# Performance work log

Measured on AMD Instinct MI355X. Metric: run time of the kernel, lower is better.

## Reference

```python
import jax, jax.numpy as jnp
import numpy as np

N = 100000   # nodes
E = 600000   # edges
F_IN = 128
F_OUT = 128


def setup_inputs() -> dict:
    key = jax.random.key(0)
    k1, k2, k3, k4 = jax.random.split(key, 4)
    x = jax.random.normal(k1, (N, F_IN), dtype=jnp.float32)
    edge_index = jax.random.randint(k2, (2, E), 0, N, dtype=jnp.int32)
    edge_wt = jnp.ones((E,), dtype=jnp.float32)  # learnable param, init ones
    # GCNConv weight (glorot-ish scale) and bias
    weight = jax.random.normal(k3, (F_IN, F_OUT), dtype=jnp.float32) / np.sqrt(F_IN).astype(np.float32)
    bias = jnp.zeros((F_OUT,), dtype=jnp.float32)
    u = jax.random.normal(k4, (F_IN,), dtype=jnp.float32)  # spectral-norm power-iter buffer
    return {"x": x, "edge_index": edge_index, "edge_wt": edge_wt,
            "weight": weight, "bias": bias, "u": u}


def _l2norm(v):
    return v / (jnp.linalg.norm(v) + 1e-12)


def reference(x, edge_index, edge_wt, weight, bias, u):
    # --- spectral norm on GCNConv weight (one power iteration, torch semantics:
    # u, v are stop-gradiented buffers; sigma = u^T W v keeps grad wrt W) ---
    W_sg = jax.lax.stop_gradient(weight)
    v = _l2norm(W_sg.T @ jax.lax.stop_gradient(u))
    u1 = _l2norm(W_sg @ v)
    sigma = u1 @ (weight @ v)
    W_sn = weight / sigma

    # --- per-edge sigmoid-weighted GCNConv with self loops + symmetric norm ---
    w = jax.nn.sigmoid(edge_wt)                      # [E]
    row, col = edge_index[0], edge_index[1]
    loop = jnp.arange(N, dtype=edge_index.dtype)
    row_a = jnp.concatenate([row, loop])             # [E+N]
    col_a = jnp.concatenate([col, loop])
    w_a = jnp.concatenate([w, jnp.ones((N,), w.dtype)])  # self-loop weight 1

    deg = jax.ops.segment_sum(w_a, col_a, num_segments=N)   # [N]
    dinv = jnp.where(deg > 0, deg ** -0.5, 0.0)
    norm = dinv[row_a] * w_a * dinv[col_a]           # [E+N]

    xw = x @ W_sn                                    # [N, F_OUT]
    msgs = norm[:, None] * xw[row_a]                 # [E+N, F_OUT] gather
    out = jax.ops.segment_sum(msgs, col_a, num_segments=N) + bias  # scatter
    return out
```

## Files before the change

### kernel.cpp

```cpp
#include <hip/hip_runtime.h>
#include <math.h>

#define F 128

typedef __bf16 bf16_t;
typedef unsigned long long u64;
typedef __attribute__((ext_vector_type(8))) bf16_t bf16x8;
typedef __attribute__((ext_vector_type(4))) bf16_t bf16x4;
typedef __attribute__((ext_vector_type(4))) float floatx4;

#define DEG_SCALE 8388608.0f
#define DEG_INV   (1.0f / 8388608.0f)

__global__ __launch_bounds__(256) void init_spec_k(const float* __restrict__ W,
                                                   const float* __restrict__ u,
                                                   bf16_t* __restrict__ Wt,
                                                   u64* __restrict__ dc, int n) {
    if (blockIdx.x == 0) {
        __shared__ float sv[F];
        __shared__ float red[F];
        __shared__ float snorm;
        __shared__ float s_is;
        int t = threadIdx.x;
        float s = 0.f;
        if (t < F) {
            for (int i = 0; i < F; ++i) s += W[i * F + t] * u[i];
            red[t] = s * s;
        }
        __syncthreads();
        if (t == 0) {
            float a = 0.f;
            for (int i = 0; i < F; ++i) a += red[i];
            snorm = sqrtf(a);
        }
        __syncthreads();
        if (t < F) sv[t] = s / (snorm + 1e-12f);
        __syncthreads();
        float s2 = 0.f;
        if (t < F) {
            for (int j = 0; j < F; ++j) s2 += W[t * F + j] * sv[j];
            red[t] = s2 * s2;
        }
        __syncthreads();
        if (t == 0) {
            float a = 0.f;
            for (int i = 0; i < F; ++i) a += red[i];
            float nt = sqrtf(a);
            float sigma = a / (nt + 1e-12f);
            s_is = 1.0f / sigma;
        }
        __syncthreads();
        if (t < F) {
            float is = s_is;
            for (int nrow = 0; nrow < F; ++nrow)
                Wt[nrow * F + t] = (bf16_t)(W[t * F + nrow] * is);
        }
    } else {
        int i = (blockIdx.x - 1) * 256 + threadIdx.x;
        if (i < n) dc[i] = 0ULL;
    }
}

#define GBM 64
#define LDK 136
__global__ __launch_bounds__(256) void count_gemm_k(const int* __restrict__ col,
                                                    const float* __restrict__ wt,
                                                    u64* __restrict__ dc, int e_cnt,
                                                    const float* __restrict__ x,
                                                    const bf16_t* __restrict__ Wt,
                                                    bf16_t* __restrict__ xwh, int nrows,
                                                    int gGemm) {
    __shared__ bf16_t As[GBM * LDK];
    int b = blockIdx.x;
    if (b >= gGemm) {
        int e = (b - gGemm) * 256 + threadIdx.x;
        if (e < e_cnt) {
            int c = col[e];
            float w = 1.0f / (1.0f + expf(-wt[e]));
            u64 pkt = (1ULL << 32) | (u64)(unsigned)rintf(w * DEG_SCALE);
            atomicAdd(dc + c, pkt);
        }
        return;
    }
    int tid = threadIdx.x;
    int rowBase = b * GBM;

    for (int i = tid; i < GBM * 32; i += 256) {
        int r = i >> 5, c4 = (i & 31) * 4;
        float4 xv = make_float4(0.f, 0.f, 0.f, 0.f);
        if (rowBase + r < nrows) xv = *(const float4*)(x + (size_t)(rowBase + r) * F + c4);
        bf16x4 v;
        v.x = (bf16_t)xv.x; v.y = (bf16_t)xv.y; v.z = (bf16_t)xv.z; v.w = (bf16_t)xv.w;
        *(bf16x4*)(As + r * LDK + c4) = v;
    }
    __syncthreads();

    int wave = tid >> 6, lane = tid & 63;
    int l16 = lane & 15, q = lane >> 4;
    int mrow = wave * 16;

    floatx4 acc[8];
#pragma unroll
    for (int nt = 0; nt < 8; ++nt) acc[nt] = (floatx4){0.f, 0.f, 0.f, 0.f};

#pragma unroll
    for (int kt = 0; kt < 4; ++kt) {
        bf16x8 a = *(bf16x8*)(As + (mrow + l16) * LDK + kt * 32 + q * 8);
#pragma unroll
        for (int nt = 0; nt < 8; ++nt) {
            bf16x8 bb = *(const bf16x8*)(Wt + (size_t)(nt * 16 + l16) * F + kt * 32 + q * 8);
            acc[nt] = __builtin_amdgcn_mfma_f32_16x16x32_bf16(a, bb, acc[nt], 0, 0, 0);
        }
    }
    __syncthreads();

#pragma unroll
    for (int nt = 0; nt < 8; ++nt) {
#pragma unroll
        for (int r = 0; r < 4; ++r)
            As[(mrow + q * 4 + r) * LDK + nt * 16 + l16] = (bf16_t)acc[nt][r];
    }
    __syncthreads();

    for (int i = tid; i < GBM * 16; i += 256) {
        int r = i >> 4, c = (i & 15) * 8;
        if (rowBase + r < nrows)
            *(bf16x8*)(xwh + (size_t)(rowBase + r) * F + c) = *(bf16x8*)(As + r * LDK + c);
    }
}

#define STILE 1024
__global__ __launch_bounds__(256) void scan1_k(const u64* __restrict__ dc,
                                               int* __restrict__ bsum,
                                               float* __restrict__ dinv, int n) {
    __shared__ int red[256];
    int t = threadIdx.x;
    int base = blockIdx.x * STILE + t * 4;
    int s = 0;
    for (int i = 0; i < 4; ++i) {
        if (base + i < n) {
            u64 v = dc[base + i];
            s += (int)(v >> 32);
            float d = 1.0f + (float)(unsigned)(v & 0xFFFFFFFFULL) * DEG_INV;
            dinv[base + i] = 1.0f / sqrtf(d);
        }
    }
    red[t] = s;
    __syncthreads();
    for (int o = 128; o > 0; o >>= 1) { if (t < o) red[t] += red[t + o]; __syncthreads(); }
    if (t == 0) bsum[blockIdx.x] = red[0];
}

__global__ __launch_bounds__(256) void scan2_k(int* __restrict__ bsum, int g,
                                               int* __restrict__ offsets, int n) {
    int t = threadIdx.x;
    if (g <= 256) {
        __shared__ int s[256];
        int v = (t < g) ? bsum[t] : 0;
        s[t] = v;
        __syncthreads();
        for (int o = 1; o < 256; o <<= 1) {
            int val = s[t];
            int add = (t >= o) ? s[t - o] : 0;
            __syncthreads();
            s[t] = val + add;
            __syncthreads();
        }
        if (t < g) bsum[t] = s[t] - v;
        if (t == g - 1) offsets[n] = s[t];
    } else if (t == 0) {
        int acc = 0;
        for (int i = 0; i < g; ++i) { int v = bsum[i]; bsum[i] = acc; acc += v; }
        offsets[n] = acc;
    }
}

__global__ __launch_bounds__(256) void scan3_k(const u64* __restrict__ dc,
                                               const int* __restrict__ bsum,
                                               int* __restrict__ offsets,
                                               int* __restrict__ cursor, int n) {
    __shared__ int sc[256];
    int t = threadIdx.x;
    int base = blockIdx.x * STILE + t * 4;
    int v[4] = {0, 0, 0, 0};
    for (int i = 0; i < 4; ++i)
        if (base + i < n) v[i] = (int)(dc[base + i] >> 32);
    int ts = v[0] + v[1] + v[2] + v[3];
    sc[t] = ts;
    __syncthreads();
    for (int o = 1; o < 256; o <<= 1) {
        int val = sc[t];
        int add = (t >= o) ? sc[t - o] : 0;
        __syncthreads();
        sc[t] = val + add;
        __syncthreads();
    }
    int run = bsum[blockIdx.x] + sc[t] - ts;
    for (int i = 0; i < 4; ++i) {
        if (base + i < n) { offsets[base + i] = run; cursor[base + i] = run; }
        run += v[i];
    }
}

__global__ __launch_bounds__(256) void fill_k(const int* __restrict__ row,
                                              const int* __restrict__ col,
                                              const float* __restrict__ wt,
                                              const float* __restrict__ dinv,
                                              int* __restrict__ cursor,
                                              int2* __restrict__ edat, int e_cnt) {
    int e = blockIdx.x * 256 + threadIdx.x;
    if (e < e_cnt) {
        int r = row[e], c = col[e];
        float w = 1.0f / (1.0f + expf(-wt[e]));
        float nv = dinv[r] * w * dinv[c];
        int p = atomicAdd(cursor + c, 1);
        edat[p] = make_int2(r, __float_as_int(nv));
    }
}

template <int MODE>
__global__ __launch_bounds__(256) void gather_t(const int* __restrict__ offsets,
                                                const int2* __restrict__ edat,
                                                const float* __restrict__ dinv,
                                                const float* __restrict__ x,
                                                const bf16_t* __restrict__ xh,
                                                const float* __restrict__ bias,
                                                float* __restrict__ out, int n) {
    int node = blockIdx.x * 4 + (threadIdx.x >> 6);
    if (node >= n) return;
    int lane = threadIdx.x & 63;
    const float2* x2 = (const float2*)x;
    float dv = dinv[node];
    float2 acc;
    if (MODE) {
        unsigned vs = ((const unsigned*)(xh + (size_t)node * F))[lane];
        acc.x = dv * dv * __uint_as_float(vs << 16);
        acc.y = dv * dv * __uint_as_float(vs & 0xFFFF0000u);
    } else {
        float2 xv = x2[(size_t)node * 64 + lane];
        acc.x = dv * dv * xv.x;
        acc.y = dv * dv * xv.y;
    }
    int s = offsets[node], e = offsets[node + 1];
    for (int b = s; b < e; b += 64) {
        int cnt = min(64, e - b);
        int2 ed = make_int2(0, 0);
        if (lane < cnt) ed = edat[b + lane];
        int j = 0;
        for (; j + 4 <= cnt; j += 4) {
            int r0 = __shfl(ed.x, j + 0), r1 = __shfl(ed.x, j + 1);
            int r2 = __shfl(ed.x, j + 2), r3 = __shfl(ed.x, j + 3);
            float n0 = __int_as_float(__shfl(ed.y, j + 0));
            float n1 = __int_as_float(__shfl(ed.y, j + 1));
            float n2 = __int_as_float(__shfl(ed.y, j + 2));
            float n3 = __int_as_float(__shfl(ed.y, j + 3));
            if (MODE) {
                unsigned v0 = ((const unsigned*)(xh + (size_t)r0 * F))[lane];
                unsigned v1 = ((const unsigned*)(xh + (size_t)r1 * F))[lane];
                unsigned v2 = ((const unsigned*)(xh + (size_t)r2 * F))[lane];
                unsigned v3 = ((const unsigned*)(xh + (size_t)r3 * F))[lane];
                acc.x = fmaf(n0, __uint_as_float(v0 << 16), acc.x);
                acc.y = fmaf(n0, __uint_as_float(v0 & 0xFFFF0000u), acc.y);
                acc.x = fmaf(n1, __uint_as_float(v1 << 16), acc.x);
                acc.y = fmaf(n1, __uint_as_float(v1 & 0xFFFF0000u), acc.y);
                acc.x = fmaf(n2, __uint_as_float(v2 << 16), acc.x);
                acc.y = fmaf(n2, __uint_as_float(v2 & 0xFFFF0000u), acc.y);
                acc.x = fmaf(n3, __uint_as_float(v3 << 16), acc.x);
                acc.y = fmaf(n3, __uint_as_float(v3 & 0xFFFF0000u), acc.y);
            } else {
                float2 a0 = x2[(size_t)r0 * 64 + lane];
                float2 a1 = x2[(size_t)r1 * 64 + lane];
                float2 a2 = x2[(size_t)r2 * 64 + lane];
                float2 a3 = x2[(size_t)r3 * 64 + lane];
                acc.x = fmaf(n0, a0.x, acc.x); acc.y = fmaf(n0, a0.y, acc.y);
                acc.x = fmaf(n1, a1.x, acc.x); acc.y = fmaf(n1, a1.y, acc.y);
                acc.x = fmaf(n2, a2.x, acc.x); acc.y = fmaf(n2, a2.y, acc.y);
                acc.x = fmaf(n3, a3.x, acc.x); acc.y = fmaf(n3, a3.y, acc.y);
            }
        }
        for (; j < cnt; ++j) {
            int r = __shfl(ed.x, j);
            float nv = __int_as_float(__shfl(ed.y, j));
            if (MODE) {
                unsigned v = ((const unsigned*)(xh + (size_t)r * F))[lane];
                acc.x = fmaf(nv, __uint_as_float(v << 16), acc.x);
                acc.y = fmaf(nv, __uint_as_float(v & 0xFFFF0000u), acc.y);
            } else {
                float2 xr = x2[(size_t)r * 64 + lane];
                acc.x = fmaf(nv, xr.x, acc.x);
                acc.y = fmaf(nv, xr.y, acc.y);
            }
        }
    }
    if (MODE) {
        float2 bv = ((const float2*)bias)[lane];
        acc.x += bv.x;
        acc.y += bv.y;
    }
    ((float2*)out)[(size_t)node * 64 + lane] = acc;
}

__global__ __launch_bounds__(256) void gemm_mfma_k(float* __restrict__ io,
                                                   const bf16_t* __restrict__ Wt,
                                                   const float* __restrict__ bias,
                                                   int nrows) {
    __shared__ bf16_t As[GBM * LDK];
    int tid = threadIdx.x;
    int rowBase = blockIdx.x * GBM;

    for (int i = tid; i < GBM * 32; i += 256) {
        int r = i >> 5, c4 = (i & 31) * 4;
        float4 xv = make_float4(0.f, 0.f, 0.f, 0.f);
        if (rowBase + r < nrows) xv = *(const float4*)(io + (size_t)(rowBase + r) * F + c4);
        bf16x4 v;
        v.x = (bf16_t)xv.x; v.y = (bf16_t)xv.y; v.z = (bf16_t)xv.z; v.w = (bf16_t)xv.w;
        *(bf16x4*)(As + r * LDK + c4) = v;
    }
    __syncthreads();

    int wave = tid >> 6, lane = tid & 63;
    int l16 = lane & 15, q = lane >> 4;
    int mrow = wave * 16;

    floatx4 acc[8];
#pragma unroll
    for (int nt = 0; nt < 8; ++nt) acc[nt] = (floatx4){0.f, 0.f, 0.f, 0.f};

#pragma unroll
    for (int kt = 0; kt < 4; ++kt) {
        bf16x8 a = *(bf16x8*)(As + (mrow + l16) * LDK + kt * 32 + q * 8);
#pragma unroll
        for (int nt = 0; nt < 8; ++nt) {
            bf16x8 b = *(const bf16x8*)(Wt + (size_t)(nt * 16 + l16) * F + kt * 32 + q * 8);
            acc[nt] = __builtin_amdgcn_mfma_f32_16x16x32_bf16(a, b, acc[nt], 0, 0, 0);
        }
    }

#pragma unroll
    for (int nt = 0; nt < 8; ++nt) {
        int col = nt * 16 + l16;
        float bv = bias[col];
#pragma unroll
        for (int r = 0; r < 4; ++r) {
            int grow = rowBase + mrow + q * 4 + r;
            if (grow < nrows) io[(size_t)grow * F + col] = acc[nt][r] + bv;
        }
    }
}

extern "C" void kernel_launch(void* const* d_in, const int* in_sizes, int n_in,
                              void* d_out, int out_size, void* d_ws, size_t ws_size,
                              hipStream_t stream) {
    const float* x    = (const float*)d_in[0];
    const int*   ei   = (const int*)d_in[1];
    const float* ewt  = (const float*)d_in[2];
    const float* W    = (const float*)d_in[3];
    const float* bias = (const float*)d_in[4];
    const float* u    = (const float*)d_in[5];
    float* out = (float*)d_out;

    int n_nodes = in_sizes[0] / F;
    int e_cnt   = in_sizes[2];
    const int* row = ei;
    const int* col = ei + e_cnt;

    char* wsb = (char*)d_ws;
    float* dinv    = (float*)wsb;
    size_t off = ((size_t)n_nodes * 4 + 15) & ~(size_t)15;
    u64*   dc      = (u64*)(wsb + off);
    off += (size_t)n_nodes * 8;
    int*   offsets = (int*)(wsb + off);
    off += (size_t)(n_nodes + 1) * 4;
    off = (off + 15) & ~(size_t)15;
    int*   cursor  = (int*)(wsb + off);
    off += (size_t)n_nodes * 4;
    int*   bsum    = (int*)(wsb + off);
    off += 512 * 4;
    off = (off + 15) & ~(size_t)15;
    int2*  edat    = (int2*)(wsb + off);
    off += (size_t)e_cnt * 8;
    off = (off + 15) & ~(size_t)15;
    bf16_t* Wt     = (bf16_t*)(wsb + off);
    off += (size_t)F * F * 2;
    bf16_t* xwh    = (bf16_t*)(wsb + off);
    size_t need_bf16 = off + (size_t)n_nodes * F * 2;
    int use_bf16 = (ws_size >= need_bf16);

    int g_scan  = (n_nodes + STILE - 1) / STILE;
    int gCount  = (e_cnt + 255) / 256;
    int gInit   = (n_nodes + 255) / 256;
    int gGemm   = (n_nodes + GBM - 1) / GBM;

    init_spec_k<<<gInit + 1, 256, 0, stream>>>(W, u, Wt, dc, n_nodes);
    if (use_bf16) {
        count_gemm_k<<<gGemm + gCount, 256, 0, stream>>>(col, ewt, dc, e_cnt, x, Wt, xwh,
                                                         n_nodes, gGemm);
    } else {
        count_gemm_k<<<gCount, 256, 0, stream>>>(col, ewt, dc, e_cnt, x, Wt, xwh,
                                                 n_nodes, 0);
    }
    scan1_k<<<g_scan, 256, 0, stream>>>(dc, bsum, dinv, n_nodes);
    scan2_k<<<1, 256, 0, stream>>>(bsum, g_scan, offsets, n_nodes);
    scan3_k<<<g_scan, 256, 0, stream>>>(dc, bsum, offsets, cursor, n_nodes);
    fill_k<<<(e_cnt + 255) / 256, 256, 0, stream>>>(row, col, ewt, dinv, cursor, edat, e_cnt);
    if (use_bf16) {
        gather_t<1><<<(n_nodes + 3) / 4, 256, 0, stream>>>(offsets, edat, dinv, x, xwh, bias,
                                                           out, n_nodes);
    } else {
        gather_t<0><<<(n_nodes + 3) / 4, 256, 0, stream>>>(offsets, edat, dinv, x, xwh, bias,
                                                           out, n_nodes);
        gemm_mfma_k<<<gGemm, 256, 0, stream>>>(out, Wt, bias, n_nodes);
    }
}
```

Baseline: 239.8 us.

## Merge degree counting into every GEMM block and stage weights in shared memory

The spectral-norm block now loads W and u into shared memory once, replaces the serial 128-element norm reductions with wave shuffles, and writes the transposed bf16 weight as vectorised 8-wide stores. The combined count/GEMM kernel no longer uses separate block ranges: each GEMM block first processes a contiguous chunk of edges for the atomic degree count, then runs its tile. A-fragments are loaded directly from global x into registers, which drops the shared-memory staging and one barrier. This reduces launch grid size and single-thread serial work, at the cost of per-block edge loops that delay the GEMM work.

```diff
diff --git a/kernel.cpp b/kernel.cpp
--- a/kernel.cpp
+++ b/kernel.cpp
@@ -17,43 +17,51 @@
                                                    bf16_t* __restrict__ Wt,
                                                    u64* __restrict__ dc, int n) {
     if (blockIdx.x == 0) {
+        __shared__ float Wl[F][F + 1];
+        __shared__ float ul[F];
         __shared__ float sv[F];
-        __shared__ float red[F];
-        __shared__ float snorm;
-        __shared__ float s_is;
+        __shared__ float red[4];
+        __shared__ float snorm, s_is;
         int t = threadIdx.x;
+        if (t < F) ul[t] = u[t];
+        for (int i = t; i < F * 32; i += 256) {
+            int r = i >> 5, c4 = (i & 31) * 4;
+            float4 v = *(const float4*)(W + r * F + c4);
+            Wl[r][c4] = v.x; Wl[r][c4 + 1] = v.y; Wl[r][c4 + 2] = v.z; Wl[r][c4 + 3] = v.w;
+        }
+        __syncthreads();
         float s = 0.f;
-        if (t < F) {
-            for (int i = 0; i < F; ++i) s += W[i * F + t] * u[i];
-            red[t] = s * s;
-        }
+        if (t < F)
+            for (int i = 0; i < F; ++i) s += Wl[i][t] * ul[i];
+        float ss = (t < F) ? s * s : 0.f;
+        for (int o = 32; o > 0; o >>= 1) ss += __shfl_down(ss, o);
+        if ((t & 63) == 0) red[t >> 6] = ss;
+        __syncthreads();
+        if (t == 0) snorm = sqrtf(red[0] + red[1] + red[2] + red[3]);
+        __syncthreads();
+        if (t < F) sv[t] = s / (snorm + 1e-12f);
+        __syncthreads();
+        float s2 = 0.f;
+        if (t < F)
+            for (int j = 0; j < F; ++j) s2 += Wl[t][j] * sv[j];
+        float ss2 = (t < F) ? s2 * s2 : 0.f;
+        for (int o = 32; o > 0; o >>= 1) ss2 += __shfl_down(ss2, o);
+        if ((t & 63) == 0) red[t >> 6] = ss2;
         __syncthreads();
         if (t == 0) {
-            float a = 0.f;
-            for (int i = 0; i < F; ++i) a += red[i];
-            snorm = sqrtf(a);
-        }
-        __syncthreads();
-        if (t < F) sv[t] = s / (snorm + 1e-12f);
-        __syncthreads();
-        float s2 = 0.f;
-        if (t < F) {
-            for (int j = 0; j < F; ++j) s2 += W[t * F + j] * sv[j];
-            red[t] = s2 * s2;
-        }
-        __syncthreads();
-        if (t == 0) {
-            float a = 0.f;
-            for (int i = 0; i < F; ++i) a += red[i];
+            float a = red[0] + red[1] + red[2] + red[3];
             float nt = sqrtf(a);
             float sigma = a / (nt + 1e-12f);
             s_is = 1.0f / sigma;
         }
         __syncthreads();
-        if (t < F) {
-            float is = s_is;
-            for (int nrow = 0; nrow < F; ++nrow)
-                Wt[nrow * F + t] = (bf16_t)(W[t * F + nrow] * is);
+        float is = s_is;
+        for (int i = t; i < F * 16; i += 256) {
+            int nrow = i >> 4, c = (i & 15) * 8;
+            bf16x8 v;
+#pragma unroll
+            for (int j = 0; j < 8; ++j) v[j] = (bf16_t)(Wl[c + j][nrow] * is);
+            *(bf16x8*)(Wt + nrow * F + c) = v;
         }
     } else {
         int i = (blockIdx.x - 1) * 256 + threadIdx.x;
@@ -69,35 +77,40 @@
                                                     const float* __restrict__ x,
                                                     const bf16_t* __restrict__ Wt,
                                                     bf16_t* __restrict__ xwh, int nrows,
-                                                    int gGemm) {
-    __shared__ bf16_t As[GBM * LDK];
-    int b = blockIdx.x;
-    if (b >= gGemm) {
-        int e = (b - gGemm) * 256 + threadIdx.x;
-        if (e < e_cnt) {
-            int c = col[e];
-            float w = 1.0f / (1.0f + expf(-wt[e]));
-            u64 pkt = (1ULL << 32) | (u64)(unsigned)rintf(w * DEG_SCALE);
-            atomicAdd(dc + c, pkt);
-        }
-        return;
-    }
-    int tid = threadIdx.x;
+                                                    int chunk) {
+    __shared__ bf16_t Os[GBM * LDK];
+    int b = blockIdx.x, tid = threadIdx.x;
+
+    int ebase = b * chunk;
+    int eend = min(ebase + chunk, e_cnt);
+    for (int e = ebase + tid; e < eend; e += 256) {
+        int c = col[e];
+        float w = 1.0f / (1.0f + expf(-wt[e]));
+        u64 pkt = (1ULL << 32) | (u64)(unsigned)rintf(w * DEG_SCALE);
+        atomicAdd(dc + c, pkt);
+    }
+    if (nrows == 0) return;
+
     int rowBase = b * GBM;
-
-    for (int i = tid; i < GBM * 32; i += 256) {
-        int r = i >> 5, c4 = (i & 31) * 4;
-        float4 xv = make_float4(0.f, 0.f, 0.f, 0.f);
-        if (rowBase + r < nrows) xv = *(const float4*)(x + (size_t)(rowBase + r) * F + c4);
-        bf16x4 v;
-        v.x = (bf16_t)xv.x; v.y = (bf16_t)xv.y; v.z = (bf16_t)xv.z; v.w = (bf16_t)xv.w;
-        *(bf16x4*)(As + r * LDK + c4) = v;
-    }
-    __syncthreads();
-
     int wave = tid >> 6, lane = tid & 63;
     int l16 = lane & 15, q = lane >> 4;
-    int mrow = wave * 16;
+    int arow = rowBase + wave * 16 + l16;
+    bool rok = (arow < nrows);
+    const float* xrow = x + (size_t)(rok ? arow : 0) * F;
+
+    bf16x8 afrag[4];
+#pragma unroll
+    for (int kt = 0; kt < 4; ++kt) {
+        float4 a0 = make_float4(0.f, 0.f, 0.f, 0.f), a1 = a0;
+        if (rok) {
+            a0 = *(const float4*)(xrow + kt * 32 + q * 8);
+            a1 = *(const float4*)(xrow + kt * 32 + q * 8 + 4);
+        }
+        bf16x8 v;
+        v[0] = (bf16_t)a0.x; v[1] = (bf16_t)a0.y; v[2] = (bf16_t)a0.z; v[3] = (bf16_t)a0.w;
+        v[4] = (bf16_t)a1.x; v[5] = (bf16_t)a1.y; v[6] = (bf16_t)a1.z; v[7] = (bf16_t)a1.w;
+        afrag[kt] = v;
+    }
 
     floatx4 acc[8];
 #pragma unroll
@@ -105,27 +118,25 @@
 
 #pragma unroll
     for (int kt = 0; kt < 4; ++kt) {
-        bf16x8 a = *(bf16x8*)(As + (mrow + l16) * LDK + kt * 32 + q * 8);
 #pragma unroll
         for (int nt = 0; nt < 8; ++nt) {
             bf16x8 bb = *(const bf16x8*)(Wt + (size_t)(nt * 16 + l16) * F + kt * 32 + q * 8);
-            acc[nt] = __builtin_amdgcn_mfma_f32_16x16x32_bf16(a, bb, acc[nt], 0, 0, 0);
-        }
-    }
-    __syncthreads();
+            acc[nt] = __builtin_amdgcn_mfma_f32_16x16x32_bf16(afrag[kt], bb, acc[nt], 0, 0, 0);
+        }
+    }
 
 #pragma unroll
     for (int nt = 0; nt < 8; ++nt) {
 #pragma unroll
         for (int r = 0; r < 4; ++r)
-            As[(mrow + q * 4 + r) * LDK + nt * 16 + l16] = (bf16_t)acc[nt][r];
+            Os[(wave * 16 + q * 4 + r) * LDK + nt * 16 + l16] = (bf16_t)acc[nt][r];
     }
     __syncthreads();
 
     for (int i = tid; i < GBM * 16; i += 256) {
         int r = i >> 4, c = (i & 15) * 8;
         if (rowBase + r < nrows)
-            *(bf16x8*)(xwh + (size_t)(rowBase + r) * F + c) = *(bf16x8*)(As + r * LDK + c);
+            *(bf16x8*)(xwh + (size_t)(rowBase + r) * F + c) = *(bf16x8*)(Os + r * LDK + c);
     }
 }
 
@@ -387,18 +398,13 @@
     int use_bf16 = (ws_size >= need_bf16);
 
     int g_scan  = (n_nodes + STILE - 1) / STILE;
-    int gCount  = (e_cnt + 255) / 256;
     int gInit   = (n_nodes + 255) / 256;
     int gGemm   = (n_nodes + GBM - 1) / GBM;
+    int chunk   = (e_cnt + gGemm - 1) / gGemm;
 
     init_spec_k<<<gInit + 1, 256, 0, stream>>>(W, u, Wt, dc, n_nodes);
-    if (use_bf16) {
-        count_gemm_k<<<gGemm + gCount, 256, 0, stream>>>(col, ewt, dc, e_cnt, x, Wt, xwh,
-                                                         n_nodes, gGemm);
-    } else {
-        count_gemm_k<<<gCount, 256, 0, stream>>>(col, ewt, dc, e_cnt, x, Wt, xwh,
-                                                 n_nodes, 0);
-    }
+    count_gemm_k<<<gGemm, 256, 0, stream>>>(col, ewt, dc, e_cnt, x, Wt, xwh,
+                                            use_bf16 ? n_nodes : 0, chunk);
     scan1_k<<<g_scan, 256, 0, stream>>>(dc, bsum, dinv, n_nodes);
     scan2_k<<<1, 256, 0, stream>>>(bsum, g_scan, offsets, n_nodes);
     scan3_k<<<g_scan, 256, 0, stream>>>(dc, bsum, offsets, cursor, n_nodes);
```

New measurement: 245.9 us. +2.5%, slower.

## Record per-edge rank from degree atomics and stage spectral-norm weight in LDS

Applied to the files above, without the earlier changes.

The degree-count atomic now returns its old count, which is saved as a per-edge rank. The CSR fill computes each slot as offsets[col]+rank instead of running a second atomic on a cursor array, so the cursor array and its writes in scan3 go away. Separately, the spectral-norm block loads W into padded shared memory, reduces with wave shuffles, and writes the transposed bf16 weight as 8-wide vectors. The cost is an extra E-sized int array written in one kernel and read in another, plus a returning atomic in the count path.

```diff
diff --git a/kernel.cpp b/kernel.cpp
--- a/kernel.cpp
+++ b/kernel.cpp
@@ -17,43 +17,51 @@
                                                    bf16_t* __restrict__ Wt,
                                                    u64* __restrict__ dc, int n) {
     if (blockIdx.x == 0) {
+        __shared__ float Wl[F][F + 1];
+        __shared__ float ul[F];
         __shared__ float sv[F];
-        __shared__ float red[F];
-        __shared__ float snorm;
-        __shared__ float s_is;
+        __shared__ float red[4];
+        __shared__ float snorm, s_is;
         int t = threadIdx.x;
+        if (t < F) ul[t] = u[t];
+        for (int i = t; i < F * 32; i += 256) {
+            int r = i >> 5, c4 = (i & 31) * 4;
+            float4 v = *(const float4*)(W + r * F + c4);
+            Wl[r][c4] = v.x; Wl[r][c4 + 1] = v.y; Wl[r][c4 + 2] = v.z; Wl[r][c4 + 3] = v.w;
+        }
+        __syncthreads();
         float s = 0.f;
-        if (t < F) {
-            for (int i = 0; i < F; ++i) s += W[i * F + t] * u[i];
-            red[t] = s * s;
-        }
+        if (t < F)
+            for (int i = 0; i < F; ++i) s += Wl[i][t] * ul[i];
+        float ss = (t < F) ? s * s : 0.f;
+        for (int o = 32; o > 0; o >>= 1) ss += __shfl_down(ss, o);
+        if ((t & 63) == 0) red[t >> 6] = ss;
+        __syncthreads();
+        if (t == 0) snorm = sqrtf(red[0] + red[1] + red[2] + red[3]);
+        __syncthreads();
+        if (t < F) sv[t] = s / (snorm + 1e-12f);
+        __syncthreads();
+        float s2 = 0.f;
+        if (t < F)
+            for (int j = 0; j < F; ++j) s2 += Wl[t][j] * sv[j];
+        float ss2 = (t < F) ? s2 * s2 : 0.f;
+        for (int o = 32; o > 0; o >>= 1) ss2 += __shfl_down(ss2, o);
+        if ((t & 63) == 0) red[t >> 6] = ss2;
         __syncthreads();
         if (t == 0) {
-            float a = 0.f;
-            for (int i = 0; i < F; ++i) a += red[i];
-            snorm = sqrtf(a);
-        }
-        __syncthreads();
-        if (t < F) sv[t] = s / (snorm + 1e-12f);
-        __syncthreads();
-        float s2 = 0.f;
-        if (t < F) {
-            for (int j = 0; j < F; ++j) s2 += W[t * F + j] * sv[j];
-            red[t] = s2 * s2;
-        }
-        __syncthreads();
-        if (t == 0) {
-            float a = 0.f;
-            for (int i = 0; i < F; ++i) a += red[i];
+            float a = red[0] + red[1] + red[2] + red[3];
             float nt = sqrtf(a);
             float sigma = a / (nt + 1e-12f);
             s_is = 1.0f / sigma;
         }
         __syncthreads();
-        if (t < F) {
-            float is = s_is;
-            for (int nrow = 0; nrow < F; ++nrow)
-                Wt[nrow * F + t] = (bf16_t)(W[t * F + nrow] * is);
+        float is = s_is;
+        for (int i = t; i < F * 16; i += 256) {
+            int nrow = i >> 4, c = (i & 15) * 8;
+            bf16x8 v;
+#pragma unroll
+            for (int j = 0; j < 8; ++j) v[j] = (bf16_t)(Wl[c + j][nrow] * is);
+            *(bf16x8*)(Wt + nrow * F + c) = v;
         }
     } else {
         int i = (blockIdx.x - 1) * 256 + threadIdx.x;
@@ -65,7 +73,8 @@
 #define LDK 136
 __global__ __launch_bounds__(256) void count_gemm_k(const int* __restrict__ col,
                                                     const float* __restrict__ wt,
-                                                    u64* __restrict__ dc, int e_cnt,
+                                                    u64* __restrict__ dc,
+                                                    int* __restrict__ rank, int e_cnt,
                                                     const float* __restrict__ x,
                                                     const bf16_t* __restrict__ Wt,
                                                     bf16_t* __restrict__ xwh, int nrows,
@@ -78,7 +87,8 @@
             int c = col[e];
             float w = 1.0f / (1.0f + expf(-wt[e]));
             u64 pkt = (1ULL << 32) | (u64)(unsigned)rintf(w * DEG_SCALE);
-            atomicAdd(dc + c, pkt);
+            u64 old = atomicAdd(dc + c, pkt);
+            rank[e] = (int)(old >> 32);
         }
         return;
     }
@@ -177,8 +187,7 @@
 
 __global__ __launch_bounds__(256) void scan3_k(const u64* __restrict__ dc,
                                                const int* __restrict__ bsum,
-                                               int* __restrict__ offsets,
-                                               int* __restrict__ cursor, int n) {
+                                               int* __restrict__ offsets, int n) {
     __shared__ int sc[256];
     int t = threadIdx.x;
     int base = blockIdx.x * STILE + t * 4;
@@ -197,7 +206,7 @@
     }
     int run = bsum[blockIdx.x] + sc[t] - ts;
     for (int i = 0; i < 4; ++i) {
-        if (base + i < n) { offsets[base + i] = run; cursor[base + i] = run; }
+        if (base + i < n) offsets[base + i] = run;
         run += v[i];
     }
 }
@@ -206,14 +215,15 @@
                                               const int* __restrict__ col,
                                               const float* __restrict__ wt,
                                               const float* __restrict__ dinv,
-                                              int* __restrict__ cursor,
+                                              const int* __restrict__ offsets,
+                                              const int* __restrict__ rank,
                                               int2* __restrict__ edat, int e_cnt) {
     int e = blockIdx.x * 256 + threadIdx.x;
     if (e < e_cnt) {
         int r = row[e], c = col[e];
         float w = 1.0f / (1.0f + expf(-wt[e]));
         float nv = dinv[r] * w * dinv[c];
-        int p = atomicAdd(cursor + c, 1);
+        int p = offsets[c] + rank[e];
         edat[p] = make_int2(r, __float_as_int(nv));
     }
 }
@@ -372,10 +382,11 @@
     int*   offsets = (int*)(wsb + off);
     off += (size_t)(n_nodes + 1) * 4;
     off = (off + 15) & ~(size_t)15;
-    int*   cursor  = (int*)(wsb + off);
-    off += (size_t)n_nodes * 4;
     int*   bsum    = (int*)(wsb + off);
     off += 512 * 4;
+    off = (off + 15) & ~(size_t)15;
+    int*   rank    = (int*)(wsb + off);
+    off += (size_t)e_cnt * 4;
     off = (off + 15) & ~(size_t)15;
     int2*  edat    = (int2*)(wsb + off);
     off += (size_t)e_cnt * 8;
@@ -393,16 +404,17 @@
 
     init_spec_k<<<gInit + 1, 256, 0, stream>>>(W, u, Wt, dc, n_nodes);
     if (use_bf16) {
-        count_gemm_k<<<gGemm + gCount, 256, 0, stream>>>(col, ewt, dc, e_cnt, x, Wt, xwh,
-                                                         n_nodes, gGemm);
+        count_gemm_k<<<gGemm + gCount, 256, 0, stream>>>(col, ewt, dc, rank, e_cnt, x, Wt,
+                                                         xwh, n_nodes, gGemm);
     } else {
-        count_gemm_k<<<gCount, 256, 0, stream>>>(col, ewt, dc, e_cnt, x, Wt, xwh,
-                                                 n_nodes, 0);
+        count_gemm_k<<<gCount, 256, 0, stream>>>(col, ewt, dc, rank, e_cnt, x, Wt,
+                                                 xwh, n_nodes, 0);
     }
     scan1_k<<<g_scan, 256, 0, stream>>>(dc, bsum, dinv, n_nodes);
     scan2_k<<<1, 256, 0, stream>>>(bsum, g_scan, offsets, n_nodes);
-    scan3_k<<<g_scan, 256, 0, stream>>>(dc, bsum, offsets, cursor, n_nodes);
-    fill_k<<<(e_cnt + 255) / 256, 256, 0, stream>>>(row, col, ewt, dinv, cursor, edat, e_cnt);
+    scan3_k<<<g_scan, 256, 0, stream>>>(dc, bsum, offsets, n_nodes);
+    fill_k<<<(e_cnt + 255) / 256, 256, 0, stream>>>(row, col, ewt, dinv, offsets, rank,
+                                                    edat, e_cnt);
     if (use_bf16) {
         gather_t<1><<<(n_nodes + 3) / 4, 256, 0, stream>>>(offsets, edat, dinv, x, xwh, bias,
                                                            out, n_nodes);
```

New measurement: 219.7 us. -8.4%, faster.
